# Performance work log

Measured on AMD Instinct MI355X. Metric: run time of the kernel, lower is better.

## Reference

```python
import jax, jax.numpy as jnp
import numpy as np


def setup_inputs() -> dict:
    key = jax.random.key(0)
    k1, k2 = jax.random.split(key, 2)
    B, H, W, C = 32, 256, 256, 32
    x = jax.random.normal(k1, (B, H, W, C), dtype=jnp.float32)
    # Dense(1) params (glorot-ish scale)
    Wm = jax.random.normal(k2, (C, 1), dtype=jnp.float32) * 0.1
    b = jnp.zeros((1,), dtype=jnp.float32)
    return {"x": x, "Wm": Wm, "b": b}


def _rotate_one(img, angle):
    # img: [H, W, C]; angle: scalar. Matches tfa.image.rotate(..., 'BILINEAR')
    # (counterclockwise rotation about image center, zero fill outside).
    H, W = img.shape[0], img.shape[1]
    dt = img.dtype
    c, s = jnp.cos(angle), jnp.sin(angle)
    w1 = jnp.asarray(W - 1, dt)
    h1 = jnp.asarray(H - 1, dt)
    # tfa angles_to_projective_transforms offsets
    x_off = (w1 - (c * w1 - s * h1)) * 0.5
    y_off = (h1 - (s * w1 + c * h1)) * 0.5
    ys, xs = jnp.meshgrid(jnp.arange(H, dtype=dt), jnp.arange(W, dtype=dt), indexing="ij")
    # output (x,y) -> input sample coords
    in_x = c * xs - s * ys + x_off  # [H, W]
    in_y = s * xs + c * ys + y_off
    x0 = jnp.floor(in_x)
    y0 = jnp.floor(in_y)
    wx = (in_x - x0)[..., None]  # [H, W, 1]
    wy = (in_y - y0)[..., None]
    x0i = x0.astype(jnp.int32)
    y0i = y0.astype(jnp.int32)
    flat = img.reshape(H * W, -1)  # [H*W, C]

    def pix(yi, xi):
        valid = (xi >= 0) & (xi < W) & (yi >= 0) & (yi < H)
        idx = jnp.clip(yi, 0, H - 1) * W + jnp.clip(xi, 0, W - 1)
        return flat[idx] * valid[..., None].astype(dt)  # [H, W, C]

    v00 = pix(y0i, x0i)
    v01 = pix(y0i, x0i + 1)
    v10 = pix(y0i + 1, x0i)
    v11 = pix(y0i + 1, x0i + 1)
    top = v00 * (1 - wx) + v01 * wx
    bot = v10 * (1 - wx) + v11 * wx
    return top * (1 - wy) + bot * wy


def reference(x, Wm, b):
    # mean-pool over spatial dims -> [B, C]
    mean_feat = jnp.mean(x, axis=(1, 2))
    pi = jnp.asarray(np.pi, x.dtype)
    angle = jnp.tanh(mean_feat @ Wm + b)[:, 0] * pi  # [B]
    angle = jnp.clip(angle, -pi, pi)
    return jax.vmap(_rotate_one)(x, angle)
```

## Files before the change

### kernel.cpp

```cpp
#include <hip/hip_runtime.h>
#include <math.h>

#define BH 256
#define BW 256
#define NB 32
#define NC 32
#define RB 64

typedef float nfloat4 __attribute__((ext_vector_type(4)));

__global__ __launch_bounds__(256) void k_reduce(const float* __restrict__ x,
                                                const float* __restrict__ Wm,
                                                float* __restrict__ partial) {
    const int b   = blockIdx.y;
    const int blk = blockIdx.x;
    const int tid = blk * 256 + threadIdx.x;
    const int threads_per_batch = RB * 256;
    const int cb = (tid * 4) & (NC - 1);
    const float w0 = Wm[cb + 0], w1 = Wm[cb + 1], w2 = Wm[cb + 2], w3 = Wm[cb + 3];

    const float4* xb = (const float4*)(x + (size_t)b * BH * BW * NC);
    const int n4 = BH * BW * NC / 4;
    float s0 = 0.f, s1 = 0.f;
    for (int i = tid; i < n4; i += 2 * threads_per_batch) {
        float4 v0 = xb[i];
        float4 v1 = xb[i + threads_per_batch];
        s0 += v0.x * w0 + v0.y * w1 + v0.z * w2 + v0.w * w3;
        s1 += v1.x * w0 + v1.y * w1 + v1.z * w2 + v1.w * w3;
    }
    float s = s0 + s1;
    for (int off = 32; off; off >>= 1) s += __shfl_down(s, off, 64);
    __shared__ float red[4];
    const int lane = threadIdx.x & 63, wv = threadIdx.x >> 6;
    if (lane == 0) red[wv] = s;
    __syncthreads();
    if (threadIdx.x == 0)
        partial[b * RB + blk] = red[0] + red[1] + red[2] + red[3];
}

__global__ void k_angle(const float* __restrict__ partial,
                        const float* __restrict__ bias,
                        float4* __restrict__ params) {
    const int b = threadIdx.x;
    if (b >= NB) return;
    float s = 0.f;
    for (int i = 0; i < RB; ++i) s += partial[b * RB + i];
    const float pi = 3.14159265358979323846f;
    float angle = tanhf(s * (1.f / (BH * BW)) + bias[0]) * pi;
    angle = fminf(fmaxf(angle, -pi), pi);
    const float cc = cosf(angle), ss = sinf(angle);
    const float w1 = (float)(BW - 1), h1 = (float)(BH - 1);
    const float xoff = (w1 - (cc * w1 - ss * h1)) * 0.5f;
    const float yoff = (h1 - (ss * w1 + cc * h1)) * 0.5f;
    params[b] = make_float4(cc, ss, xoff, yoff);
}

__global__ __launch_bounds__(256) void k_rotate(const float* __restrict__ x,
                                                const float4* __restrict__ params,
                                                float* __restrict__ out) {
    const int gid = blockIdx.x * 256 + threadIdx.x;
    const int c4  = (gid & 7) * 4;
    const int pid = gid >> 3;
    const int b   = pid >> 16;
    const int p   = pid & 65535;
    const int yo  = p >> 8;
    const int xo  = p & 255;

    const float4 prm = params[b];
    const float cc = prm.x, ss = prm.y, xoff = prm.z, yoff = prm.w;
    const float fx = (float)xo, fy = (float)yo;
    const float in_x = cc * fx - ss * fy + xoff;
    const float in_y = ss * fx + cc * fy + yoff;
    const float x0 = floorf(in_x), y0 = floorf(in_y);
    const float wx = in_x - x0, wy = in_y - y0;
    const int x0i = (int)x0, y0i = (int)y0;

    const float* xb = x + (size_t)b * (BH * BW * NC);

    auto pix = [&](int yi, int xi) -> float4 {
        const bool valid = (xi >= 0) & (xi < BW) & (yi >= 0) & (yi < BH);
        const int yc = min(max(yi, 0), BH - 1);
        const int xc = min(max(xi, 0), BW - 1);
        float4 v = *(const float4*)(xb + ((size_t)yc * BW + xc) * NC + c4);
        const float f = valid ? 1.f : 0.f;
        v.x *= f; v.y *= f; v.z *= f; v.w *= f;
        return v;
    };

    const float4 v00 = pix(y0i, x0i);
    const float4 v01 = pix(y0i, x0i + 1);
    const float4 v10 = pix(y0i + 1, x0i);
    const float4 v11 = pix(y0i + 1, x0i + 1);

    const float owx = 1.f - wx, owy = 1.f - wy;
    nfloat4 r;
    r.x = (v00.x * owx + v01.x * wx) * owy + (v10.x * owx + v11.x * wx) * wy;
    r.y = (v00.y * owx + v01.y * wx) * owy + (v10.y * owx + v11.y * wx) * wy;
    r.z = (v00.z * owx + v01.z * wx) * owy + (v10.z * owx + v11.z * wx) * wy;
    r.w = (v00.w * owx + v01.w * wx) * owy + (v10.w * owx + v11.w * wx) * wy;

    __builtin_nontemporal_store(r, (nfloat4*)(out + (size_t)gid * 4));
}

extern "C" void kernel_launch(void* const* d_in, const int* in_sizes, int n_in,
                              void* d_out, int out_size, void* d_ws, size_t ws_size,
                              hipStream_t stream) {
    const float* x    = (const float*)d_in[0];
    const float* Wm   = (const float*)d_in[1];
    const float* bias = (const float*)d_in[2];
    float* out = (float*)d_out;

    float*  partial = (float*)d_ws;
    float4* params  = (float4*)((char*)d_ws + NB * RB * sizeof(float));

    dim3 g1(RB, NB);
    k_reduce<<<g1, 256, 0, stream>>>(x, Wm, partial);
    k_angle<<<1, 64, 0, stream>>>(partial, bias, params);

    const int total4 = NB * BH * BW * NC / 4;
    k_rotate<<<total4 / 256, 256, 0, stream>>>(x, params, out);
}
```

Before: 130.8 us.

## Fuse angle computation into rotate kernel and use 2D 8x4 pixel tiles

Removes the separate single-block angle kernel: each rotate block reduces the 64 partial sums for its batch with a wave shuffle, computes the rotation parameters in thread 0 and shares them through LDS. The rotate grid is also remapped so each block covers an 8x4 spatial tile instead of a 32-pixel row strip, meant to improve cache locality of the bilinear gathers under rotation. The cost is redundant per-block tanh/sin/cos work plus a barrier in every block.

```diff
diff --git a/kernel.cpp b/kernel.cpp
--- a/kernel.cpp
+++ b/kernel.cpp
@@ -38,39 +38,43 @@
         partial[b * RB + blk] = red[0] + red[1] + red[2] + red[3];
 }
 
-__global__ void k_angle(const float* __restrict__ partial,
-                        const float* __restrict__ bias,
-                        float4* __restrict__ params) {
-    const int b = threadIdx.x;
-    if (b >= NB) return;
-    float s = 0.f;
-    for (int i = 0; i < RB; ++i) s += partial[b * RB + i];
-    const float pi = 3.14159265358979323846f;
-    float angle = tanhf(s * (1.f / (BH * BW)) + bias[0]) * pi;
-    angle = fminf(fmaxf(angle, -pi), pi);
-    const float cc = cosf(angle), ss = sinf(angle);
-    const float w1 = (float)(BW - 1), h1 = (float)(BH - 1);
-    const float xoff = (w1 - (cc * w1 - ss * h1)) * 0.5f;
-    const float yoff = (h1 - (ss * w1 + cc * h1)) * 0.5f;
-    params[b] = make_float4(cc, ss, xoff, yoff);
-}
+__global__ __launch_bounds__(256) void k_rotate(const float* __restrict__ x,
+                                                const float* __restrict__ partial,
+                                                const float* __restrict__ bias,
+                                                float* __restrict__ out) {
+    const int blk    = blockIdx.x;
+    const int b      = blk >> 11;
+    const int rem    = blk & 2047;
+    const int tile_x = rem & 31;
+    const int tile_y = rem >> 5;
 
-__global__ __launch_bounds__(256) void k_rotate(const float* __restrict__ x,
-                                                const float4* __restrict__ params,
-                                                float* __restrict__ out) {
-    const int gid = blockIdx.x * 256 + threadIdx.x;
-    const int c4  = (gid & 7) * 4;
-    const int pid = gid >> 3;
-    const int b   = pid >> 16;
-    const int p   = pid & 65535;
-    const int yo  = p >> 8;
-    const int xo  = p & 255;
+    __shared__ float4 sprm;
+    if (threadIdx.x < 64) {
+        float s = partial[b * RB + (threadIdx.x & 63)];
+        for (int off = 32; off; off >>= 1) s += __shfl_down(s, off, 64);
+        if (threadIdx.x == 0) {
+            const float pi = 3.14159265358979323846f;
+            float angle = tanhf(s * (1.f / (BH * BW)) + bias[0]) * pi;
+            angle = fminf(fmaxf(angle, -pi), pi);
+            const float cc = cosf(angle), sn = sinf(angle);
+            const float w1 = (float)(BW - 1), h1 = (float)(BH - 1);
+            const float xoff = (w1 - (cc * w1 - sn * h1)) * 0.5f;
+            const float yoff = (h1 - (sn * w1 + cc * h1)) * 0.5f;
+            sprm = make_float4(cc, sn, xoff, yoff);
+        }
+    }
+    __syncthreads();
+    const float4 prm = sprm;
 
-    const float4 prm = params[b];
-    const float cc = prm.x, ss = prm.y, xoff = prm.z, yoff = prm.w;
+    const int c4 = (threadIdx.x & 7) * 4;
+    const int px = threadIdx.x >> 3;
+    const int xo = tile_x * 8 + (px & 7);
+    const int yo = tile_y * 4 + (px >> 3);
+
+    const float cc = prm.x, sn = prm.y, xoff = prm.z, yoff = prm.w;
     const float fx = (float)xo, fy = (float)yo;
-    const float in_x = cc * fx - ss * fy + xoff;
-    const float in_y = ss * fx + cc * fy + yoff;
+    const float in_x = cc * fx - sn * fy + xoff;
+    const float in_y = sn * fx + cc * fy + yoff;
     const float x0 = floorf(in_x), y0 = floorf(in_y);
     const float wx = in_x - x0, wy = in_y - y0;
     const int x0i = (int)x0, y0i = (int)y0;
@@ -99,7 +103,8 @@
     r.z = (v00.z * owx + v01.z * wx) * owy + (v10.z * owx + v11.z * wx) * wy;
     r.w = (v00.w * owx + v01.w * wx) * owy + (v10.w * owx + v11.w * wx) * wy;
 
-    __builtin_nontemporal_store(r, (nfloat4*)(out + (size_t)gid * 4));
+    float* op = out + (((size_t)b * BH * BW + (size_t)yo * BW + xo) * NC + c4);
+    __builtin_nontemporal_store(r, (nfloat4*)op);
 }
 
 extern "C" void kernel_launch(void* const* d_in, const int* in_sizes, int n_in,
@@ -110,13 +115,11 @@
     const float* bias = (const float*)d_in[2];
     float* out = (float*)d_out;
 
-    float*  partial = (float*)d_ws;
-    float4* params  = (float4*)((char*)d_ws + NB * RB * sizeof(float));
+    float* partial = (float*)d_ws;
 
     dim3 g1(RB, NB);
     k_reduce<<<g1, 256, 0, stream>>>(x, Wm, partial);
-    k_angle<<<1, 64, 0, stream>>>(partial, bias, params);
 
-    const int total4 = NB * BH * BW * NC / 4;
-    k_rotate<<<total4 / 256, 256, 0, stream>>>(x, params, out);
+    const int nblocks = NB * 2048;
+    k_rotate<<<nblocks, 256, 0, stream>>>(x, partial, bias, out);
 }
```

New measurement: 142.4 us. +8.9%, slower.
